# Performance work log

Measured on AMD Instinct MI355X. Metric: run time of the kernel, lower is better.

## Reference

```python
import jax, jax.numpy as jnp
import numpy as np

N = 4096
D = 256
DEG = 32
E0 = N * DEG
RATIO = 0.5
NEG_SLOPE = 0.2


def setup_inputs() -> dict:
    key = jax.random.key(0)
    ks = jax.random.split(key, 12)
    # edges with NO self loops (so appending all N self-loops == add_remaining_self_loops)
    src = jax.random.randint(ks[0], (E0,), 0, N, dtype=jnp.int32)
    off = jax.random.randint(ks[1], (E0,), 1, N, dtype=jnp.int32)
    dst = ((src + off) % N).astype(jnp.int32)
    edge_index = jnp.stack([src, dst])
    edge_weight = jnp.ones((E0,), jnp.float32)
    x = jax.random.normal(ks[2], (N, D), jnp.float32)
    s = 1.0 / np.sqrt(D)
    u = lambda k, shp: jax.random.uniform(k, shp, jnp.float32, -s, s)
    return {
        'x': x,
        'edge_index': edge_index,
        'edge_weight': edge_weight,
        'lin_w': u(ks[3], (D, D)), 'lin_b': u(ks[4], (D,)),
        'att_w': jax.random.uniform(ks[5], (2 * D, 1), jnp.float32, -1.0 / np.sqrt(2 * D), 1.0 / np.sqrt(2 * D)),
        'att_b': u(ks[6], (1,)),
        'le1_w': u(ks[7], (D, 1)), 'le1_b': u(ks[8], (1,)),
        'le2_w': u(ks[9], (D, 1)),
        'le3_w': u(ks[10], (D, 1)), 'le3_b': u(ks[11], (1,)),
    }


def reference(x, edge_index, edge_weight, lin_w, lin_b, att_w, att_b,
              le1_w, le1_b, le2_w, le3_w, le3_b):
    n, d = x.shape
    # add_remaining_self_loops (input has no self loops by construction)
    loop = jnp.arange(n, dtype=edge_index.dtype)
    src = jnp.concatenate([edge_index[0], loop])
    dst = jnp.concatenate([edge_index[1], loop])
    w = jnp.concatenate([edge_weight, jnp.ones((n,), edge_weight.dtype)])

    # GNN is None -> x_pool = x
    x_pool_j = x[src]                                        # [E, D] gather
    x_q = jax.ops.segment_max(x_pool_j, dst, num_segments=n)  # scatter-max
    x_q_e = (x_q @ lin_w + lin_b)[dst]                        # [E, D]
    # att(cat([x_q, x_pool_j])) without materializing [E, 2D]
    score = x_q_e @ att_w[:d, 0] + x_pool_j @ att_w[d:, 0] + att_b[0]
    score = jax.nn.leaky_relu(score, NEG_SLOPE)
    # segment softmax over destination nodes
    smax = jax.ops.segment_max(score, dst, num_segments=n)
    ex = jnp.exp(score - smax[dst])
    denom = jax.ops.segment_sum(ex, dst, num_segments=n)
    score = ex / denom[dst]
    # dropout p=0 -> no-op
    xn = jax.ops.segment_sum(x_pool_j * score[:, None], dst, num_segments=n)

    # LEConv fitness: sigmoid( lin3(x) + sum_j (lin1(x_j) - lin2(x_i)) )
    a = xn @ le1_w + le1_b          # [N, 1]
    b = xn @ le2_w                  # [N, 1] (no bias)
    agg = jax.ops.segment_sum(a[src] - b[dst], dst, num_segments=n)
    fitness = jax.nn.sigmoid((agg + xn @ le3_w + le3_b)[:, 0])

    k = int(np.ceil(RATIO * N))
    _, perm = jax.lax.top_k(fitness, k)
    x_out = xn[perm] * fitness[perm][:, None]

    # Coarsening A_c = S[:, perm]^T @ A @ S[:, perm]; dense since SpGEMM nnz is data-dependent
    S = jnp.zeros((n, n), x.dtype).at[src, dst].add(score)[:, perm]  # [N, k]
    A = jnp.zeros((n, n), x.dtype).at[src, dst].add(w)               # [N, N]
    A_c = S.T @ (A @ S)                                              # [k, k]
    A_c = A_c * (1.0 - jnp.eye(k, dtype=A_c.dtype))                  # remove_diag
    return x_out, A_c, perm
```

## Files before the change

kernel.cpp:

```cpp
#include <hip/hip_runtime.h>
#include <cstdint>
#include <cstddef>
#include <math.h>

#define NN   4096
#define DD   256
#define E0S  131072
#define NE   (E0S + NN)
#define KK   2048
#define NEG_SLOPE 0.2f
#define SEGCAP 256

__device__ __forceinline__ int esrc(const int* s, int e){ return e < E0S ? s[e] : e - E0S; }
__device__ __forceinline__ int edst(const int* d, int e){ return e < E0S ? d[e] : e - E0S; }

__global__ void init_kernel(int* deg_dst, int* deg_src, int* colmap, float* Ac, int zero_ac){
    int i = blockIdx.x * blockDim.x + threadIdx.x;
    int stride = gridDim.x * blockDim.x;
    if (zero_ac){
        for (size_t t = i; t < (size_t)KK * KK; t += stride) Ac[t] = 0.f;
    }
    for (int t = i; t < NN; t += stride){ deg_dst[t] = 0; deg_src[t] = 0; colmap[t] = -1; }
}

__global__ void count_kernel(const int* e_src, const int* e_dst, int* deg_dst, int* deg_src){
    int e = blockIdx.x * blockDim.x + threadIdx.x;
    if (e < NE){
        atomicAdd(&deg_dst[edst(e_dst, e)], 1);
        atomicAdd(&deg_src[esrc(e_src, e)], 1);
    }
}

__global__ void __launch_bounds__(1024) scan_kernel(const int* degA, int* offA, int* curA,
                                                    const int* degB, int* offB, int* curB){
    const int* deg = (blockIdx.x == 0) ? degA : degB;
    int* off = (blockIdx.x == 0) ? offA : offB;
    int* cur = (blockIdx.x == 0) ? curA : curB;
    __shared__ int part[1024];
    int t = threadIdx.x;
    int base = t * 4;
    int s0 = deg[base], s1 = deg[base+1], s2 = deg[base+2], s3 = deg[base+3];
    int tot = s0 + s1 + s2 + s3;
    part[t] = tot;
    __syncthreads();
    for (int d = 1; d < 1024; d <<= 1){
        int v = (t >= d) ? part[t - d] : 0;
        __syncthreads();
        part[t] += v;
        __syncthreads();
    }
    int excl = part[t] - tot;
    off[base]   = excl;            cur[base]   = excl;
    off[base+1] = excl + s0;       cur[base+1] = excl + s0;
    off[base+2] = excl + s0 + s1;  cur[base+2] = excl + s0 + s1;
    off[base+3] = excl + s0 + s1 + s2; cur[base+3] = excl + s0 + s1 + s2;
    if (t == 1023) off[NN] = part[1023];
}

__global__ void fill_kernel(const int* e_src, const int* e_dst, int* cur_dst, int* cur_src,
                            int* eid_dst, int* eid_src){
    int e = blockIdx.x * blockDim.x + threadIdx.x;
    if (e < NE){
        int p = atomicAdd(&cur_dst[edst(e_dst, e)], 1); eid_dst[p] = e;
        int q = atomicAdd(&cur_src[esrc(e_src, e)], 1); eid_src[q] = e;
    }
}

__global__ void segsort_kernel(const int* off_dst, int* eid_dst, const int* off_src, int* eid_src){
    __shared__ int buf[4][SEGCAP];
    int wid  = (blockIdx.x * blockDim.x + threadIdx.x) >> 6;
    int lane = threadIdx.x & 63;
    int w    = threadIdx.x >> 6;
    const int* off; int* eid; int n;
    if (wid < NN){ off = off_dst; eid = eid_dst; n = wid; }
    else         { off = off_src; eid = eid_src; n = wid - NN; }
    int lo = off[n], hi = off[n+1];
    int L = hi - lo;
    int Lc = (L <= SEGCAP) ? L : SEGCAP;
    for (int i = lane; i < Lc; i += 64) buf[w][i] = eid[lo + i];
    __syncthreads();
    if (L <= SEGCAP){
        for (int i = lane; i < L; i += 64){
            int v = buf[w][i];
            int r = 0;
            for (int j = 0; j < L; ++j) r += (buf[w][j] < v);
            eid[lo + r] = v;
        }
    } else if (lane == 0){
        for (int i = lo + 1; i < hi; ++i){
            int v = eid[i]; int j = i - 1;
            while (j >= lo && eid[j] > v){ eid[j+1] = eid[j]; --j; }
            eid[j+1] = v;
        }
    }
}

__global__ void prepdst_kernel(const int* eid_dst, const int* e_src, int* isd){
    int u = blockIdx.x * blockDim.x + threadIdx.x;
    if (u < NE) isd[u] = esrc(e_src, eid_dst[u]);
}

__global__ void segmax_kernel(const float* x, const int* off, const int* isd, float* x_q){
    __shared__ int is_[SEGCAP];
    int n = blockIdx.x, d = threadIdx.x;
    int lo = off[n], hi = off[n+1];
    int L = hi - lo;
    int Ls = (L <= SEGCAP) ? L : SEGCAP;
    for (int t = d; t < Ls; t += 256) is_[t] = isd[lo + t];
    __syncthreads();
    float m = -INFINITY;
    int t = 0;
    for (; t + 1 < Ls; t += 2){
        float v0 = x[(size_t)is_[t]   * DD + d];
        float v1 = x[(size_t)is_[t+1] * DD + d];
        m = fmaxf(m, fmaxf(v0, v1));
    }
    if (t < Ls) m = fmaxf(m, x[(size_t)is_[t] * DD + d]);
    for (t = Ls; t < L; ++t)
        m = fmaxf(m, x[(size_t)isd[lo + t] * DD + d]);
    x_q[(size_t)n * DD + d] = m;
}

#define LROWS 8
__global__ void lin_kernel(const float* x_q, const float* w, const float* b, float* out){
    __shared__ float xs[LROWS][DD];
    int col = threadIdx.x;
    int r0 = blockIdx.x * LROWS;
    for (int r = 0; r < LROWS; ++r) xs[r][col] = x_q[(size_t)(r0 + r) * DD + col];
    __syncthreads();
    float acc[LROWS];
    float bc = b[col];
    #pragma unroll
    for (int r = 0; r < LROWS; ++r) acc[r] = bc;
    for (int kk = 0; kk < DD; ++kk){
        float wv = w[(size_t)kk * DD + col];
        #pragma unroll
        for (int r = 0; r < LROWS; ++r) acc[r] = fmaf(xs[r][kk], wv, acc[r]);
    }
    for (int r = 0; r < LROWS; ++r) out[(size_t)(r0 + r) * DD + col] = acc[r];
}

__global__ void nodedots_kernel(const float* x, const float* x_q_lin, const float* att_w,
                                float* q_s, float* p_s){
    int n = blockIdx.x, t = threadIdx.x;
    float v1 = x_q_lin[(size_t)n * DD + t] * att_w[t];
    float v2 = x[(size_t)n * DD + t] * att_w[DD + t];
    __shared__ float s1[256], s2[256];
    s1[t] = v1; s2[t] = v2;
    __syncthreads();
    for (int d = 128; d > 0; d >>= 1){
        if (t < d){ s1[t] += s1[t + d]; s2[t] += s2[t + d]; }
        __syncthreads();
    }
    if (t == 0){ q_s[n] = s1[0]; p_s[n] = s2[0]; }
}

__global__ void softmax_kernel(const int* off, const int* eid, const int* isd,
                               const float* q_s, const float* p_s, const float* att_b,
                               float* sc, float* ssd){
    int wave = threadIdx.x >> 6;
    int lane = threadIdx.x & 63;
    int n = blockIdx.x * 4 + wave;
    int lo = off[n], hi = off[n+1];
    float ab = att_b[0];
    float qn = q_s[n];
    float m = -INFINITY;
    for (int t = lo + lane; t < hi; t += 64){
        float s = qn + p_s[isd[t]] + ab;
        s = (s > 0.f) ? s : NEG_SLOPE * s;
        m = fmaxf(m, s);
    }
    #pragma unroll
    for (int d = 32; d > 0; d >>= 1) m = fmaxf(m, __shfl_xor(m, d));
    float sum = 0.f;
    for (int t = lo + lane; t < hi; t += 64){
        float s = qn + p_s[isd[t]] + ab;
        s = (s > 0.f) ? s : NEG_SLOPE * s;
        float ex = expf(s - m);
        ssd[t] = ex;
        sum += ex;
    }
    #pragma unroll
    for (int d = 32; d > 0; d >>= 1) sum += __shfl_xor(sum, d);
    float inv = 1.f / sum;
    for (int t = lo + lane; t < hi; t += 64){
        float v = ssd[t] * inv;
        ssd[t] = v;
        sc[eid[t]] = v;
    }
}

__global__ void xnfit_kernel(const float* x, const int* off, const int* isd, const float* ssd,
                             const float* le1_w, const float* le1_b, const float* le2_w,
                             const float* le3_w, const float* le3_b,
                             float* xn, float* a_, float* b_, float* c_){
    __shared__ int   is_[SEGCAP];
    __shared__ float ss_[SEGCAP];
    __shared__ float s1[256], s2[256], s3[256];
    int n = blockIdx.x, d = threadIdx.x;
    int lo = off[n], hi = off[n+1];
    int L = hi - lo;
    int Ls = (L <= SEGCAP) ? L : SEGCAP;
    for (int t = d; t < Ls; t += 256){
        is_[t] = isd[lo + t];
        ss_[t] = ssd[lo + t];
    }
    __syncthreads();
    float acc = 0.f;
    int t = 0;
    for (; t + 1 < Ls; t += 2){
        float v0 = x[(size_t)is_[t]   * DD + d];
        float v1 = x[(size_t)is_[t+1] * DD + d];
        acc = fmaf(ss_[t],   v0, acc);
        acc = fmaf(ss_[t+1], v1, acc);
    }
    if (t < Ls) acc = fmaf(ss_[t], x[(size_t)is_[t] * DD + d], acc);
    for (t = Ls; t < L; ++t)
        acc = fmaf(ssd[lo + t], x[(size_t)isd[lo + t] * DD + d], acc);
    xn[(size_t)n * DD + d] = acc;
    s1[d] = acc * le1_w[d];
    s2[d] = acc * le2_w[d];
    s3[d] = acc * le3_w[d];
    __syncthreads();
    for (int dd = 128; dd > 0; dd >>= 1){
        if (d < dd){ s1[d] += s1[d+dd]; s2[d] += s2[d+dd]; s3[d] += s3[d+dd]; }
        __syncthreads();
    }
    if (d == 0){
        a_[n] = s1[0] + le1_b[0];
        b_[n] = s2[0];
        c_[n] = s3[0] + le3_b[0];
    }
}

__global__ void fitness_kernel(const int* off, const int* isd,
                               const float* a_, const float* b_, const float* c_,
                               float* fit){
    int wave = threadIdx.x >> 6;
    int lane = threadIdx.x & 63;
    int n = blockIdx.x * 4 + wave;
    int lo = off[n], hi = off[n+1];
    float bn = b_[n];
    float s = 0.f;
    for (int t = lo + lane; t < hi; t += 64){
        s += a_[isd[t]] - bn;
    }
    #pragma unroll
    for (int d = 32; d > 0; d >>= 1) s += __shfl_xor(s, d);
    if (lane == 0){
        float z = s + c_[n];
        fit[n] = 1.f / (1.f + expf(-z));
    }
}

__global__ void __launch_bounds__(1024) topk_kernel(const float* fit, int* perm, int* colmap,
                                                    float* out_perm){
    __shared__ unsigned long long keys[NN];
    int t = threadIdx.x;
    for (int i = t; i < NN; i += 1024){
        unsigned int u = __float_as_uint(fit[i]);
        u = (u & 0x80000000u) ? ~u : (u | 0x80000000u);
        u = ~u;
        keys[i] = ((unsigned long long)u << 32) | (unsigned int)i;
    }
    __syncthreads();
    for (unsigned int ssize = 2; ssize <= NN; ssize <<= 1){
        for (unsigned int stride = ssize >> 1; stride > 0; stride >>= 1){
            for (int i = t; i < NN / 2; i += 1024){
                unsigned int idx = 2u * i - (i & (stride - 1u));
                unsigned int par = idx + stride;
                bool asc = ((idx & ssize) == 0u);
                unsigned long long a = keys[idx], b = keys[par];
                if ((a > b) == asc){ keys[idx] = b; keys[par] = a; }
            }
            __syncthreads();
        }
    }
    for (int i = t; i < KK; i += 1024){
        int node = (int)(keys[i] & 0xFFFFFFFFull);
        perm[i] = node;
        colmap[node] = i;
        out_perm[i] = (float)node;
    }
}

__global__ void xout_kernel(const float* xn, const float* fit, const int* perm, float* x_out){
    int r = blockIdx.x, d = threadIdx.x;
    int p = perm[r];
    x_out[(size_t)r * DD + d] = xn[(size_t)p * DD + d] * fit[p];
}

__global__ void colc_kernel(const int* e_dst, const int* colmap, int* colc){
    int e = blockIdx.x * blockDim.x + threadIdx.x;
    if (e < NE) colc[e] = colmap[edst(e_dst, e)];
}

__global__ void prepsrc_kernel(const int* eid_src, const int* colc, const float* sc,
                               int* cp, float* sp){
    int u = blockIdx.x * blockDim.x + threadIdx.x;
    if (u < NE){
        int f = eid_src[u];
        cp[u] = colc[f];
        sp[u] = sc[f];
    }
}

__global__ void spgemm1_kernel(const int* e_dst, const float* ew,
                               const int* off_src, const int* eid_src,
                               const int* cp, const float* sp, float* T){
    __shared__ float row[KK];
    __shared__ int   jlo_[SEGCAP];
    __shared__ int   jhi_[SEGCAP];
    __shared__ float w_[SEGCAP];
    int i = blockIdx.x;
    for (int c = threadIdx.x; c < KK; c += 256) row[c] = 0.f;
    int lo = off_src[i], hi = off_src[i+1];
    int L = hi - lo;
    int Ls = (L <= SEGCAP) ? L : SEGCAP;
    for (int t = threadIdx.x; t < Ls; t += 256){
        int e = eid_src[lo + t];
        int j = edst(e_dst, e);
        jlo_[t] = off_src[j];
        jhi_[t] = off_src[j+1];
        w_[t]   = (e < E0S) ? ew[e] : 1.0f;
    }
    __syncthreads();
    int wave = threadIdx.x >> 6, lane = threadIdx.x & 63;
    for (int t = wave; t < Ls; t += 4){
        float w1 = w_[t];
        for (int u = jlo_[t] + lane; u < jhi_[t]; u += 64){
            int c = cp[u];
            if (c >= 0) atomicAdd(&row[c], w1 * sp[u]);
        }
    }
    for (int t = Ls + wave; t < L; t += 4){
        int e = eid_src[lo + t];
        int j = edst(e_dst, e);
        float w1 = (e < E0S) ? ew[e] : 1.0f;
        int jlo = off_src[j], jhi = off_src[j+1];
        for (int u = jlo + lane; u < jhi; u += 64){
            int c = cp[u];
            if (c >= 0) atomicAdd(&row[c], w1 * sp[u]);
        }
    }
    __syncthreads();
    float* Trow = T + (size_t)i * KK;
    for (int c = threadIdx.x; c < KK; c += 256) Trow[c] = row[c];
}

__global__ void spgemm2_kernel(const int* perm, const int* off_dst,
                               const int* isd, const float* ssd,
                               const float* T, float* Ac){
    __shared__ int   is_[2][SEGCAP];
    __shared__ float ss_[2][SEGCAP];
    int bx = blockIdx.x;
    int by = blockIdx.y;
    int half = by >> 10;
    int rr   = by & 1023;
    int sub  = threadIdx.x >> 7;
    int lane = threadIdx.x & 127;
    int r = 2 * rr + sub;
    int chunk = bx + 8 * half;
    int c0 = chunk * 128 + lane;
    int node = perm[r];
    int lo = off_dst[node], hi = off_dst[node+1];
    int L = hi - lo;
    int Ls = (L <= SEGCAP) ? L : SEGCAP;
    for (int t = lane; t < Ls; t += 128){
        is_[sub][t] = isd[lo + t];
        ss_[sub][t] = ssd[lo + t];
    }
    __syncthreads();
    float acc = 0.f;
    int t = 0;
    for (; t + 3 < Ls; t += 4){
        float a0 = T[(size_t)is_[sub][t]   * KK + c0];
        float a1 = T[(size_t)is_[sub][t+1] * KK + c0];
        float a2 = T[(size_t)is_[sub][t+2] * KK + c0];
        float a3 = T[(size_t)is_[sub][t+3] * KK + c0];
        acc = fmaf(ss_[sub][t],   a0, acc);
        acc = fmaf(ss_[sub][t+1], a1, acc);
        acc = fmaf(ss_[sub][t+2], a2, acc);
        acc = fmaf(ss_[sub][t+3], a3, acc);
    }
    for (; t < Ls; ++t)
        acc = fmaf(ss_[sub][t], T[(size_t)is_[sub][t] * KK + c0], acc);
    for (t = Ls; t < L; ++t)
        acc = fmaf(ssd[lo + t], T[(size_t)isd[lo + t] * KK + c0], acc);
    float v = (c0 == r) ? 0.f : acc;
    __builtin_nontemporal_store(v, &Ac[(size_t)r * KK + c0]);
}

__global__ void ac_kernel(const int* e_src, const int* e_dst, const float* ew,
                          const int* off_src, const int* eid_src,
                          const int* colc, const float* sc, float* Ac){
    int e1 = blockIdx.x * blockDim.x + threadIdx.x;
    if (e1 >= NE) return;
    int i = (e1 < E0S) ? e_src[e1] : e1 - E0S;
    int j = (e1 < E0S) ? e_dst[e1] : e1 - E0S;
    float w1 = (e1 < E0S) ? ew[e1] : 1.0f;
    int ilo = off_src[i], ihi = off_src[i+1];
    int jlo = off_src[j], jhi = off_src[j+1];
    for (int ta = ilo; ta < ihi; ++ta){
        int ea = eid_src[ta];
        int ca = colc[ea];
        if (ca < 0) continue;
        float va = sc[ea] * w1;
        float* rowp = Ac + (size_t)ca * KK;
        for (int tb = jlo; tb < jhi; ++tb){
            int eb = eid_src[tb];
            int cb = colc[eb];
            if (cb < 0) continue;
            atomicAdd(&rowp[cb], va * sc[eb]);
        }
    }
}

__global__ void diag_kernel(float* Ac){
    int r = blockIdx.x * blockDim.x + threadIdx.x;
    if (r < KK) Ac[(size_t)r * KK + r] = 0.f;
}

extern "C" void kernel_launch(void* const* d_in, const int* in_sizes, int n_in,
                              void* d_out, int out_size, void* d_ws, size_t ws_size,
                              hipStream_t stream){
    const float* x     = (const float*)d_in[0];
    const int*   ei    = (const int*)d_in[1];
    const float* ew    = (const float*)d_in[2];
    const float* lin_w = (const float*)d_in[3];
    const float* lin_b = (const float*)d_in[4];
    const float* att_w = (const float*)d_in[5];
    const float* att_b = (const float*)d_in[6];
    const float* le1_w = (const float*)d_in[7];
    const float* le1_b = (const float*)d_in[8];
    const float* le2_w = (const float*)d_in[9];
    const float* le3_w = (const float*)d_in[10];
    const float* le3_b = (const float*)d_in[11];

    const int* e_src = ei;
    const int* e_dst = ei + E0S;

    float* out    = (float*)d_out;
    float* x_out  = out;
    float* Ac     = out + (size_t)KK * DD;
    float* operm  = out + (size_t)KK * DD + (size_t)KK * KK;

    char* wp = (char*)d_ws;
    auto alloc_i = [&](size_t n){ int* p = (int*)wp; wp += n * sizeof(int); return p; };
    auto alloc_f = [&](size_t n){ float* p = (float*)wp; wp += n * sizeof(float); return p; };

    int* deg_dst = alloc_i(NN);
    int* deg_src = alloc_i(NN);
    int* off_dst = alloc_i(NN + 1);
    int* off_src = alloc_i(NN + 1);
    int* cur_dst = alloc_i(NN);
    int* cur_src = alloc_i(NN);
    int* eid_dst = alloc_i(NE);
    int* eid_src = alloc_i(NE);
    int* colmap  = alloc_i(NN);
    int* perm    = alloc_i(KK);
    int* colc    = alloc_i(NE);
    int* isd     = alloc_i(NE);
    int* cp      = alloc_i(NE);
    float* sp    = alloc_f(NE);
    float* ssd   = alloc_f(NE);
    float* q_s   = alloc_f(NN);
    float* p_s   = alloc_f(NN);
    float* a_    = alloc_f(NN);
    float* b_    = alloc_f(NN);
    float* c_    = alloc_f(NN);
    float* fit   = alloc_f(NN);
    float* sc    = alloc_f(NE);
    float* x_q   = alloc_f((size_t)NN * DD);
    float* x_ql  = alloc_f((size_t)NN * DD);
    float* xn    = alloc_f((size_t)NN * DD);
    float* T     = alloc_f((size_t)NN * KK);
    bool dense_ok = ((size_t)(wp - (char*)d_ws) <= ws_size);
    (void)n_in; (void)in_sizes; (void)out_size;

    const int EB = (NE + 255) / 256;

    init_kernel<<<2048, 256, 0, stream>>>(deg_dst, deg_src, colmap, Ac, dense_ok ? 0 : 1);
    count_kernel<<<EB, 256, 0, stream>>>(e_src, e_dst, deg_dst, deg_src);
    scan_kernel<<<2, 1024, 0, stream>>>(deg_dst, off_dst, cur_dst, deg_src, off_src, cur_src);
    fill_kernel<<<EB, 256, 0, stream>>>(e_src, e_dst, cur_dst, cur_src, eid_dst, eid_src);
    segsort_kernel<<<(2 * NN) / 4, 256, 0, stream>>>(off_dst, eid_dst, off_src, eid_src);
    prepdst_kernel<<<EB, 256, 0, stream>>>(eid_dst, e_src, isd);
    segmax_kernel<<<NN, 256, 0, stream>>>(x, off_dst, isd, x_q);
    lin_kernel<<<NN / LROWS, 256, 0, stream>>>(x_q, lin_w, lin_b, x_ql);
    nodedots_kernel<<<NN, 256, 0, stream>>>(x, x_ql, att_w, q_s, p_s);
    softmax_kernel<<<NN / 4, 256, 0, stream>>>(off_dst, eid_dst, isd, q_s, p_s, att_b, sc, ssd);
    xnfit_kernel<<<NN, 256, 0, stream>>>(x, off_dst, isd, ssd, le1_w, le1_b, le2_w, le3_w, le3_b,
                                         xn, a_, b_, c_);
    fitness_kernel<<<NN / 4, 256, 0, stream>>>(off_dst, isd, a_, b_, c_, fit);
    topk_kernel<<<1, 1024, 0, stream>>>(fit, perm, colmap, operm);
    xout_kernel<<<KK, 256, 0, stream>>>(xn, fit, perm, x_out);
    colc_kernel<<<EB, 256, 0, stream>>>(e_dst, colmap, colc);
    if (dense_ok){
        prepsrc_kernel<<<EB, 256, 0, stream>>>(eid_src, colc, sc, cp, sp);
        spgemm1_kernel<<<NN, 256, 0, stream>>>(e_dst, ew, off_src, eid_src, cp, sp, T);
        spgemm2_kernel<<<dim3(8, KK), 256, 0, stream>>>(perm, off_dst, isd, ssd, T, Ac);
    } else {
        ac_kernel<<<EB, 256, 0, stream>>>(e_src, e_dst, ew, off_src, eid_src, colc, sc, Ac);
        diag_kernel<<<(KK + 255) / 256, 256, 0, stream>>>(Ac);
    }
}
```

Before: 243.1 us.

## Fuse isd and colc prep into neighbors and vectorize spgemm2 with float4 loads

Folds the prepdst pass into segsort, so each sorted destination edge writes its source index directly. Folds colc into prepsrc, which now reads colmap through the edge destination. Both changes drop two elementwise kernels and one NE-sized intermediate array. spgemm2 is restructured so each 32-lane group handles one output row with float4 loads and stores over 4 columns, giving 8 rows per block and a quarter of the blocks. This trades fewer, wider memory transactions for more registers per thread and less column parallelism per row.

```diff
diff --git a/kernel.cpp b/kernel.cpp
--- a/kernel.cpp
+++ b/kernel.cpp
@@ -10,6 +10,8 @@
 #define KK   2048
 #define NEG_SLOPE 0.2f
 #define SEGCAP 256
+
+typedef float floatx4 __attribute__((ext_vector_type(4)));
 
 __device__ __forceinline__ int esrc(const int* s, int e){ return e < E0S ? s[e] : e - E0S; }
 __device__ __forceinline__ int edst(const int* d, int e){ return e < E0S ? d[e] : e - E0S; }
@@ -66,14 +68,15 @@
     }
 }
 
-__global__ void segsort_kernel(const int* off_dst, int* eid_dst, const int* off_src, int* eid_src){
+__global__ void segsort_kernel(const int* off_dst, int* eid_dst, const int* off_src, int* eid_src,
+                               const int* e_src, int* isd){
     __shared__ int buf[4][SEGCAP];
     int wid  = (blockIdx.x * blockDim.x + threadIdx.x) >> 6;
     int lane = threadIdx.x & 63;
     int w    = threadIdx.x >> 6;
-    const int* off; int* eid; int n;
-    if (wid < NN){ off = off_dst; eid = eid_dst; n = wid; }
-    else         { off = off_src; eid = eid_src; n = wid - NN; }
+    const int* off; int* eid; int n; bool isdst;
+    if (wid < NN){ off = off_dst; eid = eid_dst; n = wid; isdst = true; }
+    else         { off = off_src; eid = eid_src; n = wid - NN; isdst = false; }
     int lo = off[n], hi = off[n+1];
     int L = hi - lo;
     int Lc = (L <= SEGCAP) ? L : SEGCAP;
@@ -85,6 +88,7 @@
             int r = 0;
             for (int j = 0; j < L; ++j) r += (buf[w][j] < v);
             eid[lo + r] = v;
+            if (isdst) isd[lo + r] = esrc(e_src, v);
         }
     } else if (lane == 0){
         for (int i = lo + 1; i < hi; ++i){
@@ -92,12 +96,8 @@
             while (j >= lo && eid[j] > v){ eid[j+1] = eid[j]; --j; }
             eid[j+1] = v;
         }
-    }
-}
-
-__global__ void prepdst_kernel(const int* eid_dst, const int* e_src, int* isd){
-    int u = blockIdx.x * blockDim.x + threadIdx.x;
-    if (u < NE) isd[u] = esrc(e_src, eid_dst[u]);
+        if (isdst) for (int i = lo; i < hi; ++i) isd[i] = esrc(e_src, eid[i]);
+    }
 }
 
 __global__ void segmax_kernel(const float* x, const int* off, const int* isd, float* x_q){
@@ -290,17 +290,12 @@
     x_out[(size_t)r * DD + d] = xn[(size_t)p * DD + d] * fit[p];
 }
 
-__global__ void colc_kernel(const int* e_dst, const int* colmap, int* colc){
-    int e = blockIdx.x * blockDim.x + threadIdx.x;
-    if (e < NE) colc[e] = colmap[edst(e_dst, e)];
-}
-
-__global__ void prepsrc_kernel(const int* eid_src, const int* colc, const float* sc,
-                               int* cp, float* sp){
+__global__ void prepsrc_kernel(const int* eid_src, const int* e_dst, const int* colmap,
+                               const float* sc, int* cp, float* sp){
     int u = blockIdx.x * blockDim.x + threadIdx.x;
     if (u < NE){
         int f = eid_src[u];
-        cp[u] = colc[f];
+        cp[u] = colmap[edst(e_dst, f)];
         sp[u] = sc[f];
     }
 }
@@ -351,49 +346,61 @@
 __global__ void spgemm2_kernel(const int* perm, const int* off_dst,
                                const int* isd, const float* ssd,
                                const float* T, float* Ac){
-    __shared__ int   is_[2][SEGCAP];
-    __shared__ float ss_[2][SEGCAP];
+    __shared__ int   is_[8][SEGCAP];
+    __shared__ float ss_[8][SEGCAP];
     int bx = blockIdx.x;
     int by = blockIdx.y;
-    int half = by >> 10;
-    int rr   = by & 1023;
-    int sub  = threadIdx.x >> 7;
-    int lane = threadIdx.x & 127;
-    int r = 2 * rr + sub;
+    int half = by >> 8;
+    int rr   = by & 255;
+    int sub  = threadIdx.x >> 5;
+    int lane = threadIdx.x & 31;
+    int r = rr * 8 + sub;
     int chunk = bx + 8 * half;
-    int c0 = chunk * 128 + lane;
+    int c0 = chunk * 128 + lane * 4;
     int node = perm[r];
     int lo = off_dst[node], hi = off_dst[node+1];
     int L = hi - lo;
     int Ls = (L <= SEGCAP) ? L : SEGCAP;
-    for (int t = lane; t < Ls; t += 128){
+    for (int t = lane; t < Ls; t += 32){
         is_[sub][t] = isd[lo + t];
         ss_[sub][t] = ssd[lo + t];
     }
     __syncthreads();
-    float acc = 0.f;
+    floatx4 acc = {0.f, 0.f, 0.f, 0.f};
     int t = 0;
-    for (; t + 3 < Ls; t += 4){
-        float a0 = T[(size_t)is_[sub][t]   * KK + c0];
-        float a1 = T[(size_t)is_[sub][t+1] * KK + c0];
-        float a2 = T[(size_t)is_[sub][t+2] * KK + c0];
-        float a3 = T[(size_t)is_[sub][t+3] * KK + c0];
-        acc = fmaf(ss_[sub][t],   a0, acc);
-        acc = fmaf(ss_[sub][t+1], a1, acc);
-        acc = fmaf(ss_[sub][t+2], a2, acc);
-        acc = fmaf(ss_[sub][t+3], a3, acc);
-    }
-    for (; t < Ls; ++t)
-        acc = fmaf(ss_[sub][t], T[(size_t)is_[sub][t] * KK + c0], acc);
-    for (t = Ls; t < L; ++t)
-        acc = fmaf(ssd[lo + t], T[(size_t)isd[lo + t] * KK + c0], acc);
-    float v = (c0 == r) ? 0.f : acc;
-    __builtin_nontemporal_store(v, &Ac[(size_t)r * KK + c0]);
+    for (; t + 1 < Ls; t += 2){
+        floatx4 a = *(const floatx4*)&T[(size_t)is_[sub][t]   * KK + c0];
+        floatx4 b = *(const floatx4*)&T[(size_t)is_[sub][t+1] * KK + c0];
+        float s0 = ss_[sub][t], s1 = ss_[sub][t+1];
+        acc.x = fmaf(s0, a.x, acc.x); acc.y = fmaf(s0, a.y, acc.y);
+        acc.z = fmaf(s0, a.z, acc.z); acc.w = fmaf(s0, a.w, acc.w);
+        acc.x = fmaf(s1, b.x, acc.x); acc.y = fmaf(s1, b.y, acc.y);
+        acc.z = fmaf(s1, b.z, acc.z); acc.w = fmaf(s1, b.w, acc.w);
+    }
+    for (; t < Ls; ++t){
+        floatx4 a = *(const floatx4*)&T[(size_t)is_[sub][t] * KK + c0];
+        float s0 = ss_[sub][t];
+        acc.x = fmaf(s0, a.x, acc.x); acc.y = fmaf(s0, a.y, acc.y);
+        acc.z = fmaf(s0, a.z, acc.z); acc.w = fmaf(s0, a.w, acc.w);
+    }
+    for (t = Ls; t < L; ++t){
+        floatx4 a = *(const floatx4*)&T[(size_t)isd[lo + t] * KK + c0];
+        float s0 = ssd[lo + t];
+        acc.x = fmaf(s0, a.x, acc.x); acc.y = fmaf(s0, a.y, acc.y);
+        acc.z = fmaf(s0, a.z, acc.z); acc.w = fmaf(s0, a.w, acc.w);
+    }
+    if (r - c0 >= 0 && r - c0 < 4){
+        if (r - c0 == 0) acc.x = 0.f;
+        else if (r - c0 == 1) acc.y = 0.f;
+        else if (r - c0 == 2) acc.z = 0.f;
+        else acc.w = 0.f;
+    }
+    __builtin_nontemporal_store(acc, (floatx4*)&Ac[(size_t)r * KK + c0]);
 }
 
 __global__ void ac_kernel(const int* e_src, const int* e_dst, const float* ew,
-                          const int* off_src, const int* eid_src,
-                          const int* colc, const float* sc, float* Ac){
+                          const int* off_src,
+                          const int* cp, const float* sp, float* Ac){
     int e1 = blockIdx.x * blockDim.x + threadIdx.x;
     if (e1 >= NE) return;
     int i = (e1 < E0S) ? e_src[e1] : e1 - E0S;
@@ -402,16 +409,14 @@
     int ilo = off_src[i], ihi = off_src[i+1];
     int jlo = off_src[j], jhi = off_src[j+1];
     for (int ta = ilo; ta < ihi; ++ta){
-        int ea = eid_src[ta];
-        int ca = colc[ea];
+        int ca = cp[ta];
         if (ca < 0) continue;
-        float va = sc[ea] * w1;
+        float va = sp[ta] * w1;
         float* rowp = Ac + (size_t)ca * KK;
         for (int tb = jlo; tb < jhi; ++tb){
-            int eb = eid_src[tb];
-            int cb = colc[eb];
+            int cb = cp[tb];
             if (cb < 0) continue;
-            atomicAdd(&rowp[cb], va * sc[eb]);
+            atomicAdd(&rowp[cb], va * sp[tb]);
         }
     }
 }
@@ -459,7 +464,6 @@
     int* eid_src = alloc_i(NE);
     int* colmap  = alloc_i(NN);
     int* perm    = alloc_i(KK);
-    int* colc    = alloc_i(NE);
     int* isd     = alloc_i(NE);
     int* cp      = alloc_i(NE);
     float* sp    = alloc_f(NE);
@@ -484,8 +488,7 @@
     count_kernel<<<EB, 256, 0, stream>>>(e_src, e_dst, deg_dst, deg_src);
     scan_kernel<<<2, 1024, 0, stream>>>(deg_dst, off_dst, cur_dst, deg_src, off_src, cur_src);
     fill_kernel<<<EB, 256, 0, stream>>>(e_src, e_dst, cur_dst, cur_src, eid_dst, eid_src);
-    segsort_kernel<<<(2 * NN) / 4, 256, 0, stream>>>(off_dst, eid_dst, off_src, eid_src);
-    prepdst_kernel<<<EB, 256, 0, stream>>>(eid_dst, e_src, isd);
+    segsort_kernel<<<(2 * NN) / 4, 256, 0, stream>>>(off_dst, eid_dst, off_src, eid_src, e_src, isd);
     segmax_kernel<<<NN, 256, 0, stream>>>(x, off_dst, isd, x_q);
     lin_kernel<<<NN / LROWS, 256, 0, stream>>>(x_q, lin_w, lin_b, x_ql);
     nodedots_kernel<<<NN, 256, 0, stream>>>(x, x_ql, att_w, q_s, p_s);
@@ -495,13 +498,12 @@
     fitness_kernel<<<NN / 4, 256, 0, stream>>>(off_dst, isd, a_, b_, c_, fit);
     topk_kernel<<<1, 1024, 0, stream>>>(fit, perm, colmap, operm);
     xout_kernel<<<KK, 256, 0, stream>>>(xn, fit, perm, x_out);
-    colc_kernel<<<EB, 256, 0, stream>>>(e_dst, colmap, colc);
+    prepsrc_kernel<<<EB, 256, 0, stream>>>(eid_src, e_dst, colmap, sc, cp, sp);
     if (dense_ok){
-        prepsrc_kernel<<<EB, 256, 0, stream>>>(eid_src, colc, sc, cp, sp);
         spgemm1_kernel<<<NN, 256, 0, stream>>>(e_dst, ew, off_src, eid_src, cp, sp, T);
-        spgemm2_kernel<<<dim3(8, KK), 256, 0, stream>>>(perm, off_dst, isd, ssd, T, Ac);
+        spgemm2_kernel<<<dim3(8, 512), 256, 0, stream>>>(perm, off_dst, isd, ssd, T, Ac);
     } else {
-        ac_kernel<<<EB, 256, 0, stream>>>(e_src, e_dst, ew, off_src, eid_src, colc, sc, Ac);
+        ac_kernel<<<EB, 256, 0, stream>>>(e_src, e_dst, ew, off_src, cp, sp, Ac);
         diag_kernel<<<(KK + 255) / 256, 256, 0, stream>>>(Ac);
     }
 }
```

Result: faster. 228.4 us (-6.0%).
